# Kernel optimization log

Hardware: AMD Instinct MI355X
Metric: run time of the kernel (lower is better)

## Reference

```python
import jax, jax.numpy as jnp
import numpy as np

EMBED = 512
HEADS = 8
DIM_HEAD = 64
SCALE = DIM_HEAD ** -0.5


def setup_inputs() -> dict:
    key = jax.random.key(0)
    k1, k2, k3 = jax.random.split(key, 3)
    x = jax.random.normal(k1, (1, EMBED, 64, 64), dtype=jnp.float32)
    # nn.Linear(embed, 3*embed) weight [out, in] -> store transposed [in, out] for x @ W
    W_qkv = jax.random.normal(k2, (EMBED, 3 * EMBED), dtype=jnp.float32) * (EMBED ** -0.5)
    b_qkv = jax.random.normal(k3, (3 * EMBED,), dtype=jnp.float32) * 0.01
    return {"x": x, "W_qkv": W_qkv, "b_qkv": b_qkv}


def reference(x, W_qkv, b_qkv):
    B, E, h, w = x.shape
    N = h * w
    # [B, E, H, W] -> [B, N, E]
    xs = x.reshape(B, E, N).transpose(0, 2, 1)
    qkv = xs @ W_qkv + b_qkv                      # [B, N, 3E]
    q, k, v = jnp.split(qkv, 3, axis=-1)          # each [B, N, E]

    def heads(t):
        return t.reshape(B, N, HEADS, DIM_HEAD).transpose(0, 2, 1, 3)  # [B, H, N, dh]

    q, k, v = heads(q), heads(k), heads(v)
    # raw (non-softmax) attention scores, materialized as in the original
    attn = jnp.einsum('bhqd,bhkd->bhqk', q, k) * SCALE  # [B, H, N, N]
    coarse_attn = attn.sum(axis=-2)                     # sum over queries -> [B, H, N]
    output = jnp.einsum('bhqk,bhkd->bhqd', attn, v)     # [B, H, N, dh]
    return coarse_attn, output
```

## Files before the change

kernel.cpp:

```cpp
#include <hip/hip_runtime.h>


#define N_TOK 4096
#define EMBED 512
#define J3    1536
#define HEADS 8
#define DH    64
#define SCALE 0.125f

typedef float  floatx4  __attribute__((ext_vector_type(4)));
typedef short  shortx8  __attribute__((ext_vector_type(8)));
typedef unsigned short ushortx4 __attribute__((ext_vector_type(4)));
typedef unsigned int u32;
typedef unsigned short ushort;

__device__ inline ushort f2bf(float f) {
    union { float f; u32 u; } x; x.f = f;
    u32 r = x.u + 0x7fffu + ((x.u >> 16) & 1u);
    return (ushort)(r >> 16);
}
__device__ inline float bf2f(ushort u) {
    union { u32 u; float f; } x; x.u = ((u32)u) << 16; return x.f;
}
__device__ static inline void async_copy16(void* lds, const void* g) {
    auto* gp = (const __attribute__((address_space(1))) u32*)g;
    auto* lp = (__attribute__((address_space(3))) u32*)lds;
    __builtin_amdgcn_global_load_lds(gp, lp, 16, 0, 0);
}
__device__ inline int permj(int j) {
    if (j < 512) return j;
    if (j < 1024) return 512 + ((j - 512) >> 6) * 128 + ((j - 512) & 63);
    return 512 + ((j - 1024) >> 6) * 128 + 64 + ((j - 1024) & 63);
}

__global__ __launch_bounds__(256) void prep(const float* __restrict__ x,
                                            const float* __restrict__ W,
                                            ushort* __restrict__ xT,
                                            ushort* __restrict__ WT,
                                            ushort* __restrict__ Wb,
                                            float* __restrict__ xsum) {
    const int t = threadIdx.x;
    int bx = blockIdx.x;
    const bool isx = bx < 64;
    const float* src = isx ? x : W;
    const int C = isx ? N_TOK : J3;
    if (!isx) bx -= 64;
    __shared__ float T[64][65];
    __shared__ float red[256];
    const int c0 = bx * 64, r0 = blockIdx.y * 64;
    #pragma unroll
    for (int k = 0; k < 16; ++k) {
        int i = t + 256 * k; int r = i >> 6, c = i & 63;
        T[r][c] = src[(size_t)(r0 + r) * C + c0 + c];
    }
    __syncthreads();
    if (isx) {
        int row = t >> 2, seg = (t & 3) * 16;
        float s = 0.f;
        #pragma unroll
        for (int cc = 0; cc < 16; ++cc) s += T[row][seg + cc];
        red[t] = s;
    }
    #pragma unroll
    for (int k = 0; k < 4; ++k) {
        int i = t + 256 * k; int cr = i >> 4, cc4 = (i & 15) * 4;
        ushortx4 o = { f2bf(T[cc4 + 0][cr]), f2bf(T[cc4 + 1][cr]),
                       f2bf(T[cc4 + 2][cr]), f2bf(T[cc4 + 3][cr]) };
        int dr = isx ? (c0 + cr) : permj(c0 + cr);
        ushort* dst = isx ? xT : WT;
        *(ushortx4*)&dst[(size_t)dr * 512 + r0 + cc4] = o;
    }
    if (!isx) {
        #pragma unroll
        for (int k = 0; k < 4; ++k) {
            int i = t + 256 * k; int rr = i >> 4, c4 = (i & 15) * 4;
            ushortx4 o = { f2bf(T[rr][c4 + 0]), f2bf(T[rr][c4 + 1]),
                           f2bf(T[rr][c4 + 2]), f2bf(T[rr][c4 + 3]) };
            *(ushortx4*)&Wb[(size_t)(r0 + rr) * J3 + c0 + c4] = o;
        }
    }
    if (isx) {
        __syncthreads();
        if ((t & 3) == 0)
            atomicAdd(&xsum[r0 + (t >> 2)], red[t] + red[t + 1] + red[t + 2] + red[t + 3]);
    }
}

__global__ __launch_bounds__(256) void kvm(const ushort* __restrict__ xT,
                                           const ushort* __restrict__ WT,
                                           const float* __restrict__ bias,
                                           float* __restrict__ Mp) {
    const int h = blockIdx.x, ch = blockIdx.y;
    const int j0 = 512 + h * 128, n0 = ch * 128;
    __shared__ __align__(16) char lds[34816];
    short* Kt = (short*)lds;
    short* Vt = (short*)(lds + 17408);
    const int t = threadIdx.x, lane = t & 63, w = t >> 6;
    const int wm = w & 1, wn = w >> 1;
    const int quad = lane >> 4, mrow = lane & 15;
    floatx4 acc[4][4] = {};

    auto stage = [&](int buf, int e0) {
        char* Ab = (char*)lds + (size_t)buf * 8192;
        char* Bb = (char*)lds + 16384 + (size_t)buf * 8192;
        #pragma unroll
        for (int s = 0; s < 2; ++s) {
            int i = t + 256 * s; int row = i >> 2, q = i & 3;
            async_copy16(Ab + (size_t)w * 1024 + (size_t)s * 4096,
                         xT + (size_t)(n0 + row) * 512 + e0 + q * 8);
            async_copy16(Bb + (size_t)w * 1024 + (size_t)s * 4096,
                         WT + (size_t)(j0 + row) * 512 + e0 + q * 8);
        }
    };
    stage(0, 0);
    __syncthreads();
    for (int step = 0; step < 16; ++step) {
        const int cur = step & 1;
        if (step < 15) stage(cur ^ 1, (step + 1) * 32);
        const short* As = (const short*)(lds + (size_t)cur * 8192);
        const short* Bs = (const short*)(lds + 16384 + (size_t)cur * 8192);
        shortx8 a[4], b[4];
        #pragma unroll
        for (int mi = 0; mi < 4; ++mi)
            a[mi] = *(const shortx8*)&As[(wm * 64 + mi * 16 + mrow) * 32 + quad * 8];
        #pragma unroll
        for (int ni = 0; ni < 4; ++ni)
            b[ni] = *(const shortx8*)&Bs[(wn * 64 + ni * 16 + mrow) * 32 + quad * 8];
        #pragma unroll
        for (int mi = 0; mi < 4; ++mi)
            #pragma unroll
            for (int ni = 0; ni < 4; ++ni)
                acc[mi][ni] = __builtin_amdgcn_mfma_f32_16x16x32_bf16(a[mi], b[ni], acc[mi][ni], 0, 0, 0);
        __syncthreads();
    }
    {
        short* ldst = (wn == 0) ? Kt : Vt;
        #pragma unroll
        for (int ni = 0; ni < 4; ++ni) {
            int cl = wn * 64 + ni * 16 + mrow;
            float bj = (cl < 64) ? bias[512 + h * 64 + cl] : bias[1024 + h * 64 + cl - 64];
            int dh = ni * 16 + mrow;
            #pragma unroll
            for (int mi = 0; mi < 4; ++mi)
                #pragma unroll
                for (int r = 0; r < 4; ++r) {
                    int tok = wm * 64 + mi * 16 + quad * 4 + r;
                    ldst[dh * 136 + tok] = (short)f2bf(acc[mi][ni][r] + bj);
                }
        }
    }
    __syncthreads();
    const int dpb = (w & 1) * 32, db = (w >> 1) * 32;
    floatx4 m[2][2] = {};
    #pragma unroll
    for (int kt = 0; kt < 4; ++kt) {
        shortx8 ka[2], vb[2];
        #pragma unroll
        for (int fi = 0; fi < 2; ++fi)
            ka[fi] = *(const shortx8*)&Kt[(dpb + fi * 16 + mrow) * 136 + kt * 32 + quad * 8];
        #pragma unroll
        for (int fj = 0; fj < 2; ++fj)
            vb[fj] = *(const shortx8*)&Vt[(db + fj * 16 + mrow) * 136 + kt * 32 + quad * 8];
        #pragma unroll
        for (int fi = 0; fi < 2; ++fi)
            #pragma unroll
            for (int fj = 0; fj < 2; ++fj)
                m[fi][fj] = __builtin_amdgcn_mfma_f32_16x16x32_bf16(ka[fi], vb[fj], m[fi][fj], 0, 0, 0);
    }
    float* mp = Mp + ((size_t)h * 32 + ch) * 4096;
    #pragma unroll
    for (int fi = 0; fi < 2; ++fi)
        #pragma unroll
        for (int fj = 0; fj < 2; ++fj)
            #pragma unroll
            for (int rr = 0; rr < 4; ++rr)
                mp[(dpb + fi * 16 + quad * 4 + rr) * 64 + db + fj * 16 + mrow] = m[fi][fj][rr];
}

__global__ __launch_bounds__(256) void reduce_build(const float* __restrict__ Mp,
                                                    const ushort* __restrict__ WT,
                                                    const ushort* __restrict__ Wb,
                                                    const float* __restrict__ bias,
                                                    const float* __restrict__ xsum,
                                                    ushort* __restrict__ PT,
                                                    float* __restrict__ rbuf) {
    const int h = blockIdx.x, part = blockIdx.y;
    const int t = threadIdx.x;
    const int dv0 = part * 16;
    __shared__ float Msub[64][17];
    __shared__ float red[256];
    __shared__ float Qs[64];
    {
        int dp = t >> 2, g = t & 3;
        floatx4 s = {0.f, 0.f, 0.f, 0.f};
        #pragma unroll 8
        for (int c = 0; c < 32; ++c)
            s += *(const floatx4*)&Mp[((size_t)(h * 32 + c)) * 4096 + dp * 64 + dv0 + g * 4];
        Msub[dp][g * 4 + 0] = s[0]; Msub[dp][g * 4 + 1] = s[1];
        Msub[dp][g * 4 + 2] = s[2]; Msub[dp][g * 4 + 3] = s[3];
    }
    {
        int jl = t >> 2, sg = t & 3;
        const ushort* wrow = WT + (size_t)(h * 64 + jl) * 512 + sg * 128;
        float qa = 0.f;
        #pragma unroll
        for (int g = 0; g < 16; ++g) {
            shortx8 wv = *(const shortx8*)(wrow + g * 8);
            #pragma unroll
            for (int u = 0; u < 8; ++u)
                qa += bf2f((ushort)wv[u]) * xsum[sg * 128 + g * 8 + u];
        }
        red[t] = qa;
    }
    __syncthreads();
    if (t < 64) Qs[t] = 4096.f * bias[h * 64 + t] + red[t * 4] + red[t * 4 + 1] + red[t * 4 + 2] + red[t * 4 + 3];
    {
        const int lane = t & 63, w = t >> 6;
        const int quad = lane >> 4, mrow = lane & 15;
        const int we0 = w * 128;
        floatx4 acc[8] = {};
        #pragma unroll
        for (int ks = 0; ks < 2; ++ks) {
            shortx8 ahi, alo;
            #pragma unroll
            for (int kq = 0; kq < 8; ++kq) {
                int dk = ks * 32 + quad * 8 + kq;
                float v = SCALE * Msub[dk][mrow];
                ushort hi = f2bf(v);
                ahi[kq] = (short)hi;
                alo[kq] = (short)f2bf(v - bf2f(hi));
            }
            #pragma unroll
            for (int ni = 0; ni < 8; ++ni) {
                shortx8 b = *(const shortx8*)(Wb + (size_t)(we0 + ni * 16 + mrow) * J3 + h * 64 + ks * 32 + quad * 8);
                acc[ni] = __builtin_amdgcn_mfma_f32_16x16x32_bf16(ahi, b, acc[ni], 0, 0, 0);
                acc[ni] = __builtin_amdgcn_mfma_f32_16x16x32_bf16(alo, b, acc[ni], 0, 0, 0);
            }
        }
        #pragma unroll
        for (int ni = 0; ni < 8; ++ni)
            #pragma unroll
            for (int rr = 0; rr < 4; ++rr)
                PT[(size_t)(h * 64 + dv0 + quad * 4 + rr) * 512 + we0 + ni * 16 + mrow] = f2bf(acc[ni][rr]);
    }
    if (t < 16) {
        float s = 0.f;
        #pragma unroll
        for (int dk = 0; dk < 64; ++dk) s += bias[h * 64 + dk] * Msub[dk][t];
        rbuf[h * 64 + dv0 + t] = SCALE * s;
    }
    __syncthreads();
    if (part == 0) {
        for (int e = t; e < 512; e += 256) {
            float s = 0.f;
            #pragma unroll
            for (int g = 0; g < 8; ++g) {
                shortx8 wv = *(const shortx8*)(Wb + (size_t)e * J3 + 512 + h * 64 + g * 8);
                #pragma unroll
                for (int u = 0; u < 8; ++u) s += bf2f((ushort)wv[u]) * Qs[g * 8 + u];
            }
            PT[(size_t)(512 + h) * 512 + e] = f2bf(SCALE * s);
        }
        if (t == 0) {
            float s = 0.f;
            #pragma unroll
            for (int dk = 0; dk < 64; ++dk) s += bias[512 + h * 64 + dk] * Qs[dk];
            rbuf[512 + h] = SCALE * s;
        }
    }
    {
        int idx = h * 4 + part;
        #pragma unroll
        for (int z = 0; z < 2; ++z) {
            int row = 520 + idx * 2 + z;
            if (row < 576) {
                PT[(size_t)row * 512 + t] = 0;
                PT[(size_t)row * 512 + 256 + t] = 0;
                if (t == 0) rbuf[row] = 0.f;
            }
        }
    }
}

__global__ __launch_bounds__(256) void outf(const ushort* __restrict__ xT,
                                            const ushort* __restrict__ PT,
                                            const float* __restrict__ rbuf,
                                            float* __restrict__ out) {
    const int c0 = blockIdx.x * 64, n0 = blockIdx.y * 128;
    const int t = threadIdx.x, lane = t & 63, w = t >> 6;
    const int wm = w & 1, wn = w >> 1;
    const int quad = lane >> 4, mrow = lane & 15;
    __shared__ __align__(16) char lds[24576];
    const int rowB = t >> 2, qb = t & 3;
    floatx4 acc[4][2] = {};

    auto stage = [&](int buf, int e0) {
        char* Ab = (char*)lds + (size_t)buf * 8192;
        char* Bb = (char*)lds + 16384 + (size_t)buf * 4096;
        #pragma unroll
        for (int s = 0; s < 2; ++s) {
            int i = t + 256 * s; int row = i >> 2, q = i & 3;
            async_copy16(Ab + (size_t)w * 1024 + (size_t)s * 4096,
                         xT + (size_t)(n0 + row) * 512 + e0 + q * 8);
        }
        async_copy16(Bb + (size_t)w * 1024,
                     PT + (size_t)(c0 + rowB) * 512 + e0 + qb * 8);
    };
    stage(0, 0);
    __syncthreads();
    for (int step = 0; step < 16; ++step) {
        const int cur = step & 1;
        if (step < 15) stage(cur ^ 1, (step + 1) * 32);
        const short* As = (const short*)(lds + (size_t)cur * 8192);
        const short* Bs = (const short*)(lds + 16384 + (size_t)cur * 4096);
        shortx8 a[4], b[2];
        #pragma unroll
        for (int mi = 0; mi < 4; ++mi)
            a[mi] = *(const shortx8*)&As[(wm * 64 + mi * 16 + mrow) * 32 + quad * 8];
        #pragma unroll
        for (int ni = 0; ni < 2; ++ni)
            b[ni] = *(const shortx8*)&Bs[(wn * 32 + ni * 16 + mrow) * 32 + quad * 8];
        #pragma unroll
        for (int mi = 0; mi < 4; ++mi)
            #pragma unroll
            for (int ni = 0; ni < 2; ++ni)
                acc[mi][ni] = __builtin_amdgcn_mfma_f32_16x16x32_bf16(a[mi], b[ni], acc[mi][ni], 0, 0, 0);
        __syncthreads();
    }
    #pragma unroll
    for (int ni = 0; ni < 2; ++ni) {
        int c = c0 + wn * 32 + ni * 16 + mrow;
        float rc = rbuf[c];
        #pragma unroll
        for (int mi = 0; mi < 4; ++mi)
            #pragma unroll
            for (int rr = 0; rr < 4; ++rr) {
                int n = n0 + wm * 64 + mi * 16 + quad * 4 + rr;
                float val = acc[mi][ni][rr] + rc;
                if (c < 512)
                    out[32768 + (size_t)(c >> 6) * 262144 + (size_t)n * 64 + (c & 63)] = val;
                else if (c < 520)
                    out[(size_t)(c - 512) * 4096 + n] = val;
            }
    }
}

extern "C" void kernel_launch(void* const* d_in, const int* in_sizes, int n_in,
                              void* d_out, int out_size, void* d_ws, size_t ws_size,
                              hipStream_t stream) {
    const float* x = (const float*)d_in[0];
    const float* W = (const float*)d_in[1];
    const float* b = (const float*)d_in[2];
    float* out = (float*)d_out;

    ushort* xT = (ushort*)d_ws;
    ushort* WT = xT + (size_t)N_TOK * EMBED;
    ushort* Wb = WT + (size_t)J3 * EMBED;
    ushort* PT = Wb + (size_t)EMBED * J3;
    float*  Mp = (float*)(PT + (size_t)576 * 512);
    float* xsum = Mp + (size_t)HEADS * 32 * 4096;
    float* rbuf = xsum + 512;

    prep<<<dim3(88, 8), 256, 0, stream>>>(x, W, xT, WT, Wb, xsum);
    kvm<<<dim3(8, 32), 256, 0, stream>>>(xT, WT, b, Mp);
    reduce_build<<<dim3(8, 4), 256, 0, stream>>>(Mp, WT, Wb, b, xsum, PT, rbuf);
    outf<<<dim3(9, 32), 256, 0, stream>>>(xT, PT, rbuf, out);
}
```

Baseline: 106.3 us.

## Fuse projection-build stage into output GEMM and atomically accumulate KV partials

Drops the separate reduce_build kernel and the bf16 copy of W. The kvm kernel now atomically accumulates per-head K^T V partials into four slices instead of 32, and each output block rebuilds its own projected weight tile in shared memory, reading fp32 W directly, before running the GEMM. The aim is to cut one launch, the intermediate global round trips, and the Wb writes. In exchange, the P tile is recomputed redundantly in every token block, the row-sum blocks run long serial GEMV loops, and the atomics rely on the workspace being zeroed beforehand.

```diff
diff --git a/kernel.cpp b/kernel.cpp
--- a/kernel.cpp
+++ b/kernel.cpp
@@ -27,6 +27,13 @@
     auto* lp = (__attribute__((address_space(3))) u32*)lds;
     __builtin_amdgcn_global_load_lds(gp, lp, 16, 0, 0);
 }
+__device__ inline shortx8 pack_bf8(const float* p) {
+    floatx4 w0 = *(const floatx4*)p; floatx4 w1 = *(const floatx4*)(p + 4);
+    shortx8 r;
+    r[0]=(short)f2bf(w0[0]); r[1]=(short)f2bf(w0[1]); r[2]=(short)f2bf(w0[2]); r[3]=(short)f2bf(w0[3]);
+    r[4]=(short)f2bf(w1[0]); r[5]=(short)f2bf(w1[1]); r[6]=(short)f2bf(w1[2]); r[7]=(short)f2bf(w1[3]);
+    return r;
+}
 __device__ inline int permj(int j) {
     if (j < 512) return j;
     if (j < 1024) return 512 + ((j - 512) >> 6) * 128 + ((j - 512) & 63);
@@ -37,7 +44,6 @@
                                             const float* __restrict__ W,
                                             ushort* __restrict__ xT,
                                             ushort* __restrict__ WT,
-                                            ushort* __restrict__ Wb,
                                             float* __restrict__ xsum) {
     const int t = threadIdx.x;
     int bx = blockIdx.x;
@@ -70,15 +76,6 @@
         ushort* dst = isx ? xT : WT;
         *(ushortx4*)&dst[(size_t)dr * 512 + r0 + cc4] = o;
     }
-    if (!isx) {
-        #pragma unroll
-        for (int k = 0; k < 4; ++k) {
-            int i = t + 256 * k; int rr = i >> 4, c4 = (i & 15) * 4;
-            ushortx4 o = { f2bf(T[rr][c4 + 0]), f2bf(T[rr][c4 + 1]),
-                           f2bf(T[rr][c4 + 2]), f2bf(T[rr][c4 + 3]) };
-            *(ushortx4*)&Wb[(size_t)(r0 + rr) * J3 + c0 + c4] = o;
-        }
-    }
     if (isx) {
         __syncthreads();
         if ((t & 3) == 0)
@@ -86,10 +83,10 @@
     }
 }
 
-__global__ __launch_bounds__(256) void kvm(const ushort* __restrict__ xT,
-                                           const ushort* __restrict__ WT,
-                                           const float* __restrict__ bias,
-                                           float* __restrict__ Mp) {
+__global__ __launch_bounds__(256) void kvmM(const ushort* __restrict__ xT,
+                                            const ushort* __restrict__ WT,
+                                            const float* __restrict__ bias,
+                                            float* __restrict__ M4) {
     const int h = blockIdx.x, ch = blockIdx.y;
     const int j0 = 512 + h * 128, n0 = ch * 128;
     __shared__ __align__(16) char lds[34816];
@@ -167,159 +164,143 @@
             for (int fj = 0; fj < 2; ++fj)
                 m[fi][fj] = __builtin_amdgcn_mfma_f32_16x16x32_bf16(ka[fi], vb[fj], m[fi][fj], 0, 0, 0);
     }
-    float* mp = Mp + ((size_t)h * 32 + ch) * 4096;
+    float* mp = M4 + (size_t)(h * 4 + (ch & 3)) * 4096;
     #pragma unroll
     for (int fi = 0; fi < 2; ++fi)
         #pragma unroll
         for (int fj = 0; fj < 2; ++fj)
             #pragma unroll
             for (int rr = 0; rr < 4; ++rr)
-                mp[(dpb + fi * 16 + quad * 4 + rr) * 64 + db + fj * 16 + mrow] = m[fi][fj][rr];
-}
-
-__global__ __launch_bounds__(256) void reduce_build(const float* __restrict__ Mp,
-                                                    const ushort* __restrict__ WT,
-                                                    const ushort* __restrict__ Wb,
-                                                    const float* __restrict__ bias,
-                                                    const float* __restrict__ xsum,
-                                                    ushort* __restrict__ PT,
-                                                    float* __restrict__ rbuf) {
-    const int h = blockIdx.x, part = blockIdx.y;
-    const int t = threadIdx.x;
-    const int dv0 = part * 16;
-    __shared__ float Msub[64][17];
-    __shared__ float red[256];
-    __shared__ float Qs[64];
-    {
-        int dp = t >> 2, g = t & 3;
-        floatx4 s = {0.f, 0.f, 0.f, 0.f};
-        #pragma unroll 8
-        for (int c = 0; c < 32; ++c)
-            s += *(const floatx4*)&Mp[((size_t)(h * 32 + c)) * 4096 + dp * 64 + dv0 + g * 4];
-        Msub[dp][g * 4 + 0] = s[0]; Msub[dp][g * 4 + 1] = s[1];
-        Msub[dp][g * 4 + 2] = s[2]; Msub[dp][g * 4 + 3] = s[3];
-    }
-    {
-        int jl = t >> 2, sg = t & 3;
-        const ushort* wrow = WT + (size_t)(h * 64 + jl) * 512 + sg * 128;
-        float qa = 0.f;
-        #pragma unroll
-        for (int g = 0; g < 16; ++g) {
-            shortx8 wv = *(const shortx8*)(wrow + g * 8);
-            #pragma unroll
-            for (int u = 0; u < 8; ++u)
-                qa += bf2f((ushort)wv[u]) * xsum[sg * 128 + g * 8 + u];
-        }
-        red[t] = qa;
-    }
-    __syncthreads();
-    if (t < 64) Qs[t] = 4096.f * bias[h * 64 + t] + red[t * 4] + red[t * 4 + 1] + red[t * 4 + 2] + red[t * 4 + 3];
-    {
-        const int lane = t & 63, w = t >> 6;
-        const int quad = lane >> 4, mrow = lane & 15;
-        const int we0 = w * 128;
-        floatx4 acc[8] = {};
-        #pragma unroll
-        for (int ks = 0; ks < 2; ++ks) {
-            shortx8 ahi, alo;
-            #pragma unroll
-            for (int kq = 0; kq < 8; ++kq) {
-                int dk = ks * 32 + quad * 8 + kq;
-                float v = SCALE * Msub[dk][mrow];
-                ushort hi = f2bf(v);
-                ahi[kq] = (short)hi;
-                alo[kq] = (short)f2bf(v - bf2f(hi));
-            }
-            #pragma unroll
-            for (int ni = 0; ni < 8; ++ni) {
-                shortx8 b = *(const shortx8*)(Wb + (size_t)(we0 + ni * 16 + mrow) * J3 + h * 64 + ks * 32 + quad * 8);
-                acc[ni] = __builtin_amdgcn_mfma_f32_16x16x32_bf16(ahi, b, acc[ni], 0, 0, 0);
-                acc[ni] = __builtin_amdgcn_mfma_f32_16x16x32_bf16(alo, b, acc[ni], 0, 0, 0);
-            }
-        }
-        #pragma unroll
-        for (int ni = 0; ni < 8; ++ni)
-            #pragma unroll
-            for (int rr = 0; rr < 4; ++rr)
-                PT[(size_t)(h * 64 + dv0 + quad * 4 + rr) * 512 + we0 + ni * 16 + mrow] = f2bf(acc[ni][rr]);
-    }
-    if (t < 16) {
-        float s = 0.f;
-        #pragma unroll
-        for (int dk = 0; dk < 64; ++dk) s += bias[h * 64 + dk] * Msub[dk][t];
-        rbuf[h * 64 + dv0 + t] = SCALE * s;
-    }
-    __syncthreads();
-    if (part == 0) {
-        for (int e = t; e < 512; e += 256) {
-            float s = 0.f;
-            #pragma unroll
-            for (int g = 0; g < 8; ++g) {
-                shortx8 wv = *(const shortx8*)(Wb + (size_t)e * J3 + 512 + h * 64 + g * 8);
-                #pragma unroll
-                for (int u = 0; u < 8; ++u) s += bf2f((ushort)wv[u]) * Qs[g * 8 + u];
-            }
-            PT[(size_t)(512 + h) * 512 + e] = f2bf(SCALE * s);
-        }
-        if (t == 0) {
-            float s = 0.f;
-            #pragma unroll
-            for (int dk = 0; dk < 64; ++dk) s += bias[512 + h * 64 + dk] * Qs[dk];
-            rbuf[512 + h] = SCALE * s;
-        }
-    }
-    {
-        int idx = h * 4 + part;
-        #pragma unroll
-        for (int z = 0; z < 2; ++z) {
-            int row = 520 + idx * 2 + z;
-            if (row < 576) {
-                PT[(size_t)row * 512 + t] = 0;
-                PT[(size_t)row * 512 + 256 + t] = 0;
-                if (t == 0) rbuf[row] = 0.f;
-            }
-        }
-    }
-}
-
-__global__ __launch_bounds__(256) void outf(const ushort* __restrict__ xT,
-                                            const ushort* __restrict__ PT,
-                                            const float* __restrict__ rbuf,
-                                            float* __restrict__ out) {
-    const int c0 = blockIdx.x * 64, n0 = blockIdx.y * 128;
+                atomicAdd(&mp[(dpb + fi * 16 + quad * 4 + rr) * 64 + db + fj * 16 + mrow], m[fi][fj][rr]);
+}
+
+__global__ __launch_bounds__(256) void outfused(const ushort* __restrict__ xT,
+                                                const float* __restrict__ W,
+                                                const float* __restrict__ bias,
+                                                const float* __restrict__ xsum,
+                                                const float* __restrict__ M4,
+                                                float* __restrict__ out) {
+    const int bx = blockIdx.x;
+    const int n0 = blockIdx.y * 128;
     const int t = threadIdx.x, lane = t & 63, w = t >> 6;
     const int wm = w & 1, wn = w >> 1;
     const int quad = lane >> 4, mrow = lane & 15;
-    __shared__ __align__(16) char lds[24576];
-    const int rowB = t >> 2, qb = t & 3;
-    floatx4 acc[4][2] = {};
-
-    auto stage = [&](int buf, int e0) {
-        char* Ab = (char*)lds + (size_t)buf * 8192;
-        char* Bb = (char*)lds + 16384 + (size_t)buf * 4096;
+    __shared__ __align__(16) char lds[99840];
+    float* MT = (float*)lds;
+    short* Pl = (short*)(lds + 16640);
+    char*  Ad = lds + 83200;
+    float* rv = (float*)(lds + 99584);
+
+    auto stageA = [&](int buf, int e0) {
+        char* Ab = Ad + (size_t)buf * 8192;
         #pragma unroll
         for (int s = 0; s < 2; ++s) {
             int i = t + 256 * s; int row = i >> 2, q = i & 3;
             async_copy16(Ab + (size_t)w * 1024 + (size_t)s * 4096,
                          xT + (size_t)(n0 + row) * 512 + e0 + q * 8);
         }
-        async_copy16(Bb + (size_t)w * 1024,
-                     PT + (size_t)(c0 + rowB) * 512 + e0 + qb * 8);
     };
-    stage(0, 0);
+    stageA(0, 0);
+
+    if (bx < 8) {
+        const int h = bx;
+        {
+            #pragma unroll
+            for (int g = 0; g < 4; ++g) {
+                int idx = t * 16 + g * 4;
+                int dk = idx >> 6, dv = idx & 63;
+                floatx4 s = {0.f, 0.f, 0.f, 0.f};
+                #pragma unroll
+                for (int c = 0; c < 4; ++c)
+                    s += *(const floatx4*)&M4[(size_t)(h * 4 + c) * 4096 + idx];
+                MT[(dv + 0) * 65 + dk] = s[0]; MT[(dv + 1) * 65 + dk] = s[1];
+                MT[(dv + 2) * 65 + dk] = s[2]; MT[(dv + 3) * 65 + dk] = s[3];
+            }
+        }
+        __syncthreads();
+        if (t < 64) {
+            float s = 0.f;
+            #pragma unroll
+            for (int dk = 0; dk < 64; ++dk) s += bias[h * 64 + dk] * MT[t * 65 + dk];
+            rv[t] = SCALE * s;
+        }
+        {
+            const int we0 = w * 128;
+            floatx4 pacc[4][8] = {};
+            #pragma unroll
+            for (int ks = 0; ks < 2; ++ks) {
+                shortx8 ahi[4], alo[4];
+                #pragma unroll
+                for (int mi = 0; mi < 4; ++mi)
+                    #pragma unroll
+                    for (int kq = 0; kq < 8; ++kq) {
+                        float v = SCALE * MT[(mi * 16 + mrow) * 65 + ks * 32 + quad * 8 + kq];
+                        ushort hi = f2bf(v);
+                        ahi[mi][kq] = (short)hi;
+                        alo[mi][kq] = (short)f2bf(v - bf2f(hi));
+                    }
+                #pragma unroll
+                for (int ni = 0; ni < 8; ++ni) {
+                    shortx8 bfr = pack_bf8(W + (size_t)(we0 + ni * 16 + mrow) * J3 + h * 64 + ks * 32 + quad * 8);
+                    #pragma unroll
+                    for (int mi = 0; mi < 4; ++mi) {
+                        pacc[mi][ni] = __builtin_amdgcn_mfma_f32_16x16x32_bf16(ahi[mi], bfr, pacc[mi][ni], 0, 0, 0);
+                        pacc[mi][ni] = __builtin_amdgcn_mfma_f32_16x16x32_bf16(alo[mi], bfr, pacc[mi][ni], 0, 0, 0);
+                    }
+                }
+            }
+            #pragma unroll
+            for (int mi = 0; mi < 4; ++mi)
+                #pragma unroll
+                for (int ni = 0; ni < 8; ++ni)
+                    #pragma unroll
+                    for (int rr = 0; rr < 4; ++rr)
+                        Pl[(mi * 16 + quad * 4 + rr) * 520 + we0 + ni * 16 + mrow] = (short)f2bf(pacc[mi][ni][rr]);
+        }
+    } else {
+        float* Qs = MT;
+        for (int j = t; j < 512; j += 256) {
+            float s = 4096.f * bias[j];
+            for (int e = 0; e < 512; ++e) s += W[(size_t)e * J3 + j] * xsum[e];
+            Qs[j] = s;
+        }
+        __syncthreads();
+        for (int e = t; e < 512; e += 256) {
+            #pragma unroll
+            for (int hh = 0; hh < 8; ++hh) {
+                float s = 0.f;
+                #pragma unroll
+                for (int dk = 0; dk < 64; ++dk)
+                    s += W[(size_t)e * J3 + 512 + hh * 64 + dk] * Qs[hh * 64 + dk];
+                Pl[hh * 520 + e] = (short)f2bf(SCALE * s);
+            }
+        }
+        for (int i = t; i < 56 * 512; i += 256) {
+            int r = 8 + (i >> 9), c = i & 511;
+            Pl[r * 520 + c] = 0;
+        }
+        if (t < 64) rv[t] = 0.f;
+        if (t < 8) {
+            float s = 0.f;
+            #pragma unroll
+            for (int dk = 0; dk < 64; ++dk) s += bias[512 + t * 64 + dk] * Qs[t * 64 + dk];
+            rv[t] = SCALE * s;
+        }
+    }
     __syncthreads();
+
+    floatx4 acc[4][2] = {};
     for (int step = 0; step < 16; ++step) {
         const int cur = step & 1;
-        if (step < 15) stage(cur ^ 1, (step + 1) * 32);
-        const short* As = (const short*)(lds + (size_t)cur * 8192);
-        const short* Bs = (const short*)(lds + 16384 + (size_t)cur * 4096);
+        if (step < 15) stageA(cur ^ 1, (step + 1) * 32);
+        const short* As = (const short*)(Ad + (size_t)cur * 8192);
         shortx8 a[4], b[2];
         #pragma unroll
         for (int mi = 0; mi < 4; ++mi)
             a[mi] = *(const shortx8*)&As[(wm * 64 + mi * 16 + mrow) * 32 + quad * 8];
         #pragma unroll
         for (int ni = 0; ni < 2; ++ni)
-            b[ni] = *(const shortx8*)&Bs[(wn * 32 + ni * 16 + mrow) * 32 + quad * 8];
+            b[ni] = *(const shortx8*)&Pl[(wn * 32 + ni * 16 + mrow) * 520 + step * 32 + quad * 8];
         #pragma unroll
         for (int mi = 0; mi < 4; ++mi)
             #pragma unroll
@@ -329,18 +310,18 @@
     }
     #pragma unroll
     for (int ni = 0; ni < 2; ++ni) {
-        int c = c0 + wn * 32 + ni * 16 + mrow;
-        float rc = rbuf[c];
+        int cl = wn * 32 + ni * 16 + mrow;
+        float rc = rv[cl];
         #pragma unroll
         for (int mi = 0; mi < 4; ++mi)
             #pragma unroll
             for (int rr = 0; rr < 4; ++rr) {
                 int n = n0 + wm * 64 + mi * 16 + quad * 4 + rr;
                 float val = acc[mi][ni][rr] + rc;
-                if (c < 512)
-                    out[32768 + (size_t)(c >> 6) * 262144 + (size_t)n * 64 + (c & 63)] = val;
-                else if (c < 520)
-                    out[(size_t)(c - 512) * 4096 + n] = val;
+                if (bx < 8)
+                    out[32768 + (size_t)bx * 262144 + (size_t)n * 64 + cl] = val;
+                else if (cl < 8)
+                    out[(size_t)cl * 4096 + n] = val;
             }
     }
 }
@@ -355,14 +336,10 @@
 
     ushort* xT = (ushort*)d_ws;
     ushort* WT = xT + (size_t)N_TOK * EMBED;
-    ushort* Wb = WT + (size_t)J3 * EMBED;
-    ushort* PT = Wb + (size_t)EMBED * J3;
-    float*  Mp = (float*)(PT + (size_t)576 * 512);
-    float* xsum = Mp + (size_t)HEADS * 32 * 4096;
-    float* rbuf = xsum + 512;
-
-    prep<<<dim3(88, 8), 256, 0, stream>>>(x, W, xT, WT, Wb, xsum);
-    kvm<<<dim3(8, 32), 256, 0, stream>>>(xT, WT, b, Mp);
-    reduce_build<<<dim3(8, 4), 256, 0, stream>>>(Mp, WT, Wb, b, xsum, PT, rbuf);
-    outf<<<dim3(9, 32), 256, 0, stream>>>(xT, PT, rbuf, out);
-}
+    float*  M4 = (float*)(WT + (size_t)J3 * EMBED);
+    float* xsum = M4 + (size_t)HEADS * 4 * 4096;
+
+    prep<<<dim3(88, 8), 256, 0, stream>>>(x, W, xT, WT, xsum);
+    kvmM<<<dim3(8, 32), 256, 0, stream>>>(xT, WT, b, M4);
+    outfused<<<dim3(9, 32), 256, 0, stream>>>(xT, W, b, xsum, M4, out);
+}
```

Measured after the change: 205.5 us. 1.93x slower.
